# Kernel optimization log

Measured on AMD Instinct MI355X. Metric: run time of the kernel, lower is better.

Reference implementation:

```python
import jax, jax.numpy as jnp
import numpy as np

N = 100000          # num nodes
NUM_GRAPHS = 64
NEG_SLOPE = 0.2     # PyG GATv2Conv default


def gatv2_layer(x, src, dst, Wl, bl, Wr, br, att, bias, heads, out_ch, concat):
    # x: [N, F_in]; src/dst: [E] (self-loops already included)
    xl = (x @ Wl + bl).reshape(-1, heads, out_ch)   # source transform
    xr = (x @ Wr + br).reshape(-1, heads, out_ch)   # target transform
    m = jax.nn.leaky_relu(xl[src] + xr[dst], NEG_SLOPE)      # [E, H, C]
    alpha = jnp.einsum('ehc,hc->eh', m, att)                 # [E, H]
    # segment softmax over destination nodes
    amax = jax.ops.segment_max(alpha, dst, num_segments=N)
    alpha = jnp.exp(alpha - amax[dst])
    denom = jax.ops.segment_sum(alpha, dst, num_segments=N)
    alpha = alpha / (denom[dst] + 1e-16)
    out = jax.ops.segment_sum(xl[src] * alpha[..., None], dst, num_segments=N)
    out = out.reshape(N, heads * out_ch) if concat else out.mean(axis=1)
    return out + bias


def setup_inputs() -> dict:
    key = jax.random.key(0)
    ks = jax.random.split(key, 16)
    E = 3200000
    x = jax.random.normal(ks[0], (N, 256), dtype=jnp.float32)
    edge_index = jax.random.randint(ks[1], (2, E), 0, N, dtype=jnp.int64)
    batch = jnp.sort(jax.random.randint(ks[2], (N,), 0, NUM_GRAPHS, dtype=jnp.int64))
    H1, C1 = 8, 4
    s1 = 1.0 / np.sqrt(256)
    s2 = 1.0 / np.sqrt(H1 * C1)
    return {
        'x': x, 'edge_index': edge_index, 'batch': batch,
        'W1l': jax.random.normal(ks[3], (256, H1 * C1), jnp.float32) * s1,
        'b1l': jnp.zeros((H1 * C1,), jnp.float32),
        'W1r': jax.random.normal(ks[4], (256, H1 * C1), jnp.float32) * s1,
        'b1r': jnp.zeros((H1 * C1,), jnp.float32),
        'att1': jax.random.normal(ks[5], (H1, C1), jnp.float32),
        'bias1': jnp.zeros((H1 * C1,), jnp.float32),
        'W2l': jax.random.normal(ks[6], (H1 * C1, 64), jnp.float32) * s2,
        'b2l': jnp.zeros((64,), jnp.float32),
        'W2r': jax.random.normal(ks[7], (H1 * C1, 64), jnp.float32) * s2,
        'b2r': jnp.zeros((64,), jnp.float32),
        'att2': jax.random.normal(ks[8], (1, 64), jnp.float32),
        'bias2': jnp.zeros((64,), jnp.float32),
    }


def reference(x, edge_index, batch, W1l, b1l, W1r, b1r, att1, bias1,
              W2l, b2l, W2r, b2r, att2, bias2):
    # add self-loops (PyG GATv2Conv default add_self_loops=True)
    loop = jnp.arange(N, dtype=edge_index.dtype)
    src = jnp.concatenate([edge_index[0], loop])
    dst = jnp.concatenate([edge_index[1], loop])
    h = gatv2_layer(x, src, dst, W1l, b1l, W1r, b1r, att1, bias1, 8, 4, True)
    h = jax.nn.elu(h)
    h = gatv2_layer(h, src, dst, W2l, b2l, W2r, b2r, att2, bias2, 1, 64, False)
    # global mean pool over graphs
    sums = jax.ops.segment_sum(h, batch, num_segments=NUM_GRAPHS)
    counts = jax.ops.segment_sum(jnp.ones((N, 1), h.dtype), batch, num_segments=NUM_GRAPHS)
    return sums / jnp.maximum(counts, 1.0)
```

## Files before the change

### kernel.cpp

```cpp
#include <hip/hip_runtime.h>
#include <math.h>

#define NN 100000
#define EE 3200000
#define ET (EE + NN)
#define NG 64

#define NB 196
#define BWID 512
#define PCHUNK 8192
#define PBLOCKS ((ET + PCHUNK - 1) / PCHUNK)

#define X1_SPLIT 50048
#define X1BLK_A 391
#define X1BLK_B 391

#define OFF_XL1B  0u
#define OFF_XR1   1600000u
#define OFF_HL2B  8000000u
#define OFF_HR2   11200000u
#define OFF_BEDGE 8000000u
#define OFF_RP    17600000u
#define OFF_ESRC  17700096u
#define OFF_POOL  21000096u
#define OFF_CNTG  21004192u
#define OFF_BCNT  21004256u
#define OFF_BOFF  21004512u
#define OFF_GCUR  21004768u
#define OFF_AL2   21005024u
#define OFF_AR2   21105024u
#define WS_UNITS  21205024u

__device__ __forceinline__ float lrelu(float v) { return fmaxf(v, 0.2f * v); }

__device__ __forceinline__ unsigned pack_bf2(float a, float b) {
  unsigned ua = __float_as_uint(a), ub = __float_as_uint(b);
  ua = (ua + 0x7FFFu + ((ua >> 16) & 1u)) >> 16;
  ub = (ub + 0x7FFFu + ((ub >> 16) & 1u)) & 0xFFFF0000u;
  return ua | ub;
}
__device__ __forceinline__ float bf_lo(unsigned u) { return __uint_as_float(u << 16); }
__device__ __forceinline__ float bf_hi(unsigned u) { return __uint_as_float(u & 0xFFFF0000u); }

__global__ __launch_bounds__(256) void k_bcount(const int* __restrict__ ei,
                                                int* __restrict__ bcnt) {
  __shared__ int h[NB];
  for (int i = threadIdx.x; i < NB; i += 256) h[i] = 0;
  __syncthreads();
  for (long e = (long)blockIdx.x * 256 + threadIdx.x; e < ET; e += (long)gridDim.x * 256) {
    int d = (e < EE) ? ei[EE + e] : (int)(e - EE);
    atomicAdd(&h[d >> 9], 1);
  }
  __syncthreads();
  for (int i = threadIdx.x; i < NB; i += 256) if (h[i]) atomicAdd(&bcnt[i], h[i]);
}

__global__ __launch_bounds__(256) void k_bscan(const int* __restrict__ bcnt,
                                               int* __restrict__ boff, int* __restrict__ gcur) {
  __shared__ int sd[256];
  int t = threadIdx.x;
  int v = (t < NB) ? bcnt[t] : 0;
  sd[t] = v;
  __syncthreads();
  for (int o = 1; o < 256; o <<= 1) {
    int u = (t >= o) ? sd[t - o] : 0;
    __syncthreads();
    sd[t] += u;
    __syncthreads();
  }
  if (t < NB) { boff[t] = sd[t] - v; gcur[t] = sd[t] - v; }
  if (t == 0) boff[NB] = ET;
}

__device__ void part_role(char* smem, const int* __restrict__ ei,
                          int* __restrict__ gcur, int* __restrict__ bedge, int pblk) {
  int* cnt   = (int*)smem;
  int* lbase = cnt + NB;
  int* gbase = lbase + NB;
  int* sc    = gbase + NB;
  int* buf   = sc + 256;
  unsigned char* bkt = (unsigned char*)(buf + PCHUNK);
  int tid = threadIdx.x;
  long e0 = (long)pblk * PCHUNK;
  int nedge = (e0 + PCHUNK <= ET) ? PCHUNK : (int)(ET - e0);

  for (int i = tid; i < NB; i += 512) cnt[i] = 0;
  __syncthreads();
  for (int i = tid; i < nedge; i += 512) {
    long e = e0 + i;
    int d = (e < EE) ? ei[EE + e] : (int)(e - EE);
    atomicAdd(&cnt[d >> 9], 1);
  }
  __syncthreads();
  if (tid < 256) sc[tid] = (tid < NB) ? cnt[tid] : 0;
  __syncthreads();
  for (int o = 1; o < 256; o <<= 1) {
    int u = (tid < 256 && tid >= o) ? sc[tid - o] : 0;
    __syncthreads();
    if (tid < 256) sc[tid] += u;
    __syncthreads();
  }
  if (tid < NB) lbase[tid] = sc[tid] - cnt[tid];
  __syncthreads();
  if (tid < NB) {
    int c = cnt[tid];
    gbase[tid] = c ? atomicAdd(&gcur[tid], c) : 0;
    cnt[tid] = 0;
  }
  __syncthreads();
  for (int i = tid; i < nedge; i += 512) {
    long e = e0 + i;
    int s, d;
    if (e < EE) { s = ei[e]; d = ei[EE + e]; }
    else { s = (int)(e - EE); d = s; }
    int b = d >> 9;
    int r = atomicAdd(&cnt[b], 1);
    int idx = lbase[b] + r;
    buf[idx] = s | ((d & 511) << 17);
    bkt[idx] = (unsigned char)b;
  }
  __syncthreads();
  for (int i = tid; i < nedge; i += 512) {
    int p = buf[i];
    int b = bkt[i];
    bedge[gbase[b] + (i - lbase[b])] = p;
  }
}

__device__ void csr_role(char* smem, const int* __restrict__ boff,
                         const int* __restrict__ bedge,
                         int* __restrict__ rp, int* __restrict__ esrc, int b) {
  int* sdeg  = (int*)smem;
  int* sscan = sdeg + BWID;
  int t = threadIdx.x;
  int n0 = b * BWID;
  int lo = boff[b], hi = boff[b + 1];
  sdeg[t] = 0;
  __syncthreads();
  for (int i = lo + t; i < hi; i += 512) {
    int p = bedge[i];
    atomicAdd(&sdeg[p >> 17], 1);
  }
  __syncthreads();
  int v = sdeg[t];
  sscan[t] = v;
  __syncthreads();
  for (int o = 1; o < 512; o <<= 1) {
    int u = (t >= o) ? sscan[t - o] : 0;
    __syncthreads();
    sscan[t] += u;
    __syncthreads();
  }
  int excl = sscan[t] - v;
  int n = n0 + t;
  if (n < NN) rp[n] = lo + excl;
  if (b == NB - 1 && t == 0) rp[NN] = ET;
  __syncthreads();
  sdeg[t] = lo + excl;
  __syncthreads();
  for (int i = lo + t; i < hi; i += 512) {
    int p = bedge[i];
    int pos = atomicAdd(&sdeg[p >> 17], 1);
    esrc[pos] = p & 0x1FFFF;
  }
}

#define FMA4A(a, xv) \
  a.x += xv.x*w0.x + xv.y*w1.x + xv.z*w2.x + xv.w*w3.x; \
  a.y += xv.x*w0.y + xv.y*w1.y + xv.z*w2.y + xv.w*w3.y; \
  a.z += xv.x*w0.z + xv.y*w1.z + xv.z*w2.z + xv.w*w3.z; \
  a.w += xv.x*w0.w + xv.y*w1.w + xv.z*w2.w + xv.w*w3.w;

__device__ void xform1_role(char* smem, const float* __restrict__ x,
                            const float* __restrict__ Wl, const float* __restrict__ bl,
                            const float* __restrict__ Wr, const float* __restrict__ br,
                            unsigned short* __restrict__ xl1b, float* __restrict__ xr1,
                            int n_base) {
  float* Wlds = (float*)smem;
  int tid = threadIdx.x;
  int ci = tid & 15;
  int cbase = ci * 4;
  int n0 = n_base + (tid >> 4) * 4;
  int r0 = n0 + 0 < NN ? n0 + 0 : NN - 1;
  int r1 = n0 + 1 < NN ? n0 + 1 : NN - 1;
  int r2 = n0 + 2 < NN ? n0 + 2 : NN - 1;
  int r3 = n0 + 3 < NN ? n0 + 3 : NN - 1;
  const float* xb0 = x + (size_t)r0 * 256;
  const float* xb1 = x + (size_t)r1 * 256;
  const float* xb2 = x + (size_t)r2 * 256;
  const float* xb3 = x + (size_t)r3 * 256;
  float4 acc0 = {0,0,0,0}, acc1 = {0,0,0,0}, acc2 = {0,0,0,0}, acc3 = {0,0,0,0};

  for (int q = 0; q < 4; ++q) {
    int k0 = q * 64;
    __syncthreads();
    for (int i = tid; i < 64 * 64; i += 512) {
      int k = (i >> 6) + k0, c = i & 63;
      Wlds[i] = (c < 32) ? Wl[k * 32 + c] : Wr[k * 32 + (c - 32)];
    }
    __syncthreads();
#pragma unroll 2
    for (int kk = 0; kk < 64; kk += 4) {
      int k = k0 + kk;
      float4 xv0 = *(const float4*)(xb0 + k);
      float4 xv1 = *(const float4*)(xb1 + k);
      float4 xv2 = *(const float4*)(xb2 + k);
      float4 xv3 = *(const float4*)(xb3 + k);
      const float* wr = &Wlds[kk * 64 + cbase];
      float4 w0 = *(const float4*)(wr);
      float4 w1 = *(const float4*)(wr + 64);
      float4 w2 = *(const float4*)(wr + 128);
      float4 w3 = *(const float4*)(wr + 192);
      FMA4A(acc0, xv0)
      FMA4A(acc1, xv1)
      FMA4A(acc2, xv2)
      FMA4A(acc3, xv3)
    }
  }
  float4 acc[4] = {acc0, acc1, acc2, acc3};
  if (cbase < 32) {
    float4 bv = { bl[cbase], bl[cbase+1], bl[cbase+2], bl[cbase+3] };
#pragma unroll
    for (int j = 0; j < 4; ++j) {
      int n = n0 + j;
      if (n < NN) {
        uint2 o = { pack_bf2(acc[j].x + bv.x, acc[j].y + bv.y),
                    pack_bf2(acc[j].z + bv.z, acc[j].w + bv.w) };
        *(uint2*)(xl1b + (size_t)n * 32 + cbase) = o;
      }
    }
  } else {
    int c2 = cbase - 32;
    float4 bv = { br[c2], br[c2+1], br[c2+2], br[c2+3] };
#pragma unroll
    for (int j = 0; j < 4; ++j) {
      int n = n0 + j;
      if (n < NN) {
        float4 o = { acc[j].x + bv.x, acc[j].y + bv.y, acc[j].z + bv.z, acc[j].w + bv.w };
        *(float4*)(xr1 + (size_t)n * 32 + c2) = o;
      }
    }
  }
}

__global__ __launch_bounds__(512) void k_part_x1(
    const int* __restrict__ ei, int* __restrict__ gcur, int* __restrict__ bedge,
    const float* __restrict__ x,
    const float* __restrict__ Wl, const float* __restrict__ bl,
    const float* __restrict__ Wr, const float* __restrict__ br,
    unsigned short* __restrict__ xl1b, float* __restrict__ xr1) {
  extern __shared__ char smem[];
  if (blockIdx.x < PBLOCKS)
    part_role(smem, ei, gcur, bedge, blockIdx.x);
  else
    xform1_role(smem, x, Wl, bl, Wr, br, xl1b, xr1, (blockIdx.x - PBLOCKS) * 128);
}

__global__ __launch_bounds__(512) void k_csr_x1(
    const int* __restrict__ boff, const int* __restrict__ bedge,
    int* __restrict__ rp, int* __restrict__ esrc,
    const float* __restrict__ x,
    const float* __restrict__ Wl, const float* __restrict__ bl,
    const float* __restrict__ Wr, const float* __restrict__ br,
    unsigned short* __restrict__ xl1b, float* __restrict__ xr1) {
  extern __shared__ char smem[];
  if (blockIdx.x < NB)
    csr_role(smem, boff, bedge, rp, esrc, blockIdx.x);
  else
    xform1_role(smem, x, Wl, bl, Wr, br, xl1b, xr1,
                X1_SPLIT + (blockIdx.x - NB) * 128);
}

__global__ __launch_bounds__(256) void k_gather1x2(
    const int* __restrict__ rp, const int* __restrict__ esrc,
    const unsigned short* __restrict__ xl1b, const float* __restrict__ xr1,
    const float* __restrict__ att1, const float* __restrict__ bias1,
    const float* __restrict__ W2l, const float* __restrict__ b2l,
    const float* __restrict__ W2r, const float* __restrict__ b2r,
    const float* __restrict__ att2,
    unsigned short* __restrict__ hl2b, float* __restrict__ hr2,
    float* __restrict__ AL2, float* __restrict__ AR2) {
  __shared__ float W2lds[32 * 128];
  __shared__ float hlds[8][33];
  int tid = threadIdx.x;
  for (int i = tid; i < 32 * 128; i += 256) {
    int k = i >> 7, c = i & 127;
    W2lds[i] = (c < 64) ? W2l[k * 64 + c] : W2r[k * 64 + (c - 64)];
  }
  int n = blockIdx.x * 8 + (tid >> 5);
  int l = tid & 31;
  float av = att1[l];
  float xr = xr1[(size_t)n * 32 + l];
  int rpn = rp[n], dg = rp[n + 1] - rpn;
  float acc = 0.0f, den = 0.0f;
  int j = 0;
  for (; j + 4 <= dg; j += 4) {
    int s0 = esrc[rpn + j + 0];
    int s1 = esrc[rpn + j + 1];
    int s2 = esrc[rpn + j + 2];
    int s3 = esrc[rpn + j + 3];
    float x0 = bf_lo(xl1b[(size_t)s0 * 32 + l]);
    float x1 = bf_lo(xl1b[(size_t)s1 * 32 + l]);
    float x2 = bf_lo(xl1b[(size_t)s2 * 32 + l]);
    float x3 = bf_lo(xl1b[(size_t)s3 * 32 + l]);
    float p0 = lrelu(x0 + xr) * av;
    float p1 = lrelu(x1 + xr) * av;
    float p2 = lrelu(x2 + xr) * av;
    float p3 = lrelu(x3 + xr) * av;
    p0 += __shfl_xor(p0, 1); p1 += __shfl_xor(p1, 1);
    p2 += __shfl_xor(p2, 1); p3 += __shfl_xor(p3, 1);
    p0 += __shfl_xor(p0, 2); p1 += __shfl_xor(p1, 2);
    p2 += __shfl_xor(p2, 2); p3 += __shfl_xor(p3, 2);
    float w0 = __expf(p0), w1 = __expf(p1), w2 = __expf(p2), w3 = __expf(p3);
    den += w0 + w1 + w2 + w3;
    acc += w0 * x0 + w1 * x1 + w2 * x2 + w3 * x3;
  }
  for (; j < dg; ++j) {
    int s = esrc[rpn + j];
    float xl = bf_lo(xl1b[(size_t)s * 32 + l]);
    float p = lrelu(xl + xr) * av;
    p += __shfl_xor(p, 1);
    p += __shfl_xor(p, 2);
    float w = __expf(p);
    den += w;
    acc += w * xl;
  }
  float v = acc / (den + 1e-16f) + bias1[l];
  v = v > 0.0f ? v : expm1f(v);
  hlds[tid >> 5][l] = v;
  __syncthreads();

  int ni = tid >> 5, ci = tid & 31, cbase = ci * 4;
  float4 a = {0,0,0,0};
#pragma unroll
  for (int k = 0; k < 32; ++k) {
    float hv = hlds[ni][k];
    float4 wv = *(const float4*)(&W2lds[k * 128 + cbase]);
    a.x += hv * wv.x; a.y += hv * wv.y; a.z += hv * wv.z; a.w += hv * wv.w;
  }
  int no = blockIdx.x * 8 + ni;
  float partial;
  if (cbase < 64) {
    uint2 o = { pack_bf2(a.x + b2l[cbase], a.y + b2l[cbase + 1]),
                pack_bf2(a.z + b2l[cbase + 2], a.w + b2l[cbase + 3]) };
    *(uint2*)(hl2b + (size_t)no * 64 + cbase) = o;
    partial = bf_lo(o.x) * att2[cbase + 0] + bf_hi(o.x) * att2[cbase + 1]
            + bf_lo(o.y) * att2[cbase + 2] + bf_hi(o.y) * att2[cbase + 3];
  } else {
    int c2 = cbase - 64;
    float4 o = { a.x + b2r[c2], a.y + b2r[c2 + 1], a.z + b2r[c2 + 2], a.w + b2r[c2 + 3] };
    *(float4*)(hr2 + (size_t)no * 64 + c2) = o;
    partial = o.x * att2[c2 + 0] + o.y * att2[c2 + 1]
            + o.z * att2[c2 + 2] + o.w * att2[c2 + 3];
  }
  partial += __shfl_xor(partial, 1);
  partial += __shfl_xor(partial, 2);
  partial += __shfl_xor(partial, 4);
  partial += __shfl_xor(partial, 8);
  if (ci == 0)  AL2[no] = partial;
  if (ci == 16) AR2[no] = partial;
}

#define G2_P(qq, pp) { \
  float4 U0 = { bf_lo(qq.x), bf_hi(qq.x), bf_lo(qq.y), bf_hi(qq.y) }; \
  float4 U1 = { bf_lo(qq.z), bf_hi(qq.z), bf_lo(qq.w), bf_hi(qq.w) }; \
  pp = fabsf(U0.x + hr0.x) * ac0.x + fabsf(U0.y + hr0.y) * ac0.y \
     + fabsf(U0.z + hr0.z) * ac0.z + fabsf(U0.w + hr0.w) * ac0.w \
     + fabsf(U1.x + hr1.x) * ac1.x + fabsf(U1.y + hr1.y) * ac1.y \
     + fabsf(U1.z + hr1.z) * ac1.z + fabsf(U1.w + hr1.w) * ac1.w; }

#define G2_ACC(qq, ww) { \
  float4 U0 = { bf_lo(qq.x), bf_hi(qq.x), bf_lo(qq.y), bf_hi(qq.y) }; \
  float4 U1 = { bf_lo(qq.z), bf_hi(qq.z), bf_lo(qq.w), bf_hi(qq.w) }; \
  a0.x += ww * U0.x; a0.y += ww * U0.y; a0.z += ww * U0.z; a0.w += ww * U0.w; \
  a1.x += ww * U1.x; a1.y += ww * U1.y; a1.z += ww * U1.z; a1.w += ww * U1.w; }

__global__ __launch_bounds__(256) void k_gather2(
    const int* __restrict__ rp, const int* __restrict__ esrc,
    const unsigned short* __restrict__ hl2b, const float* __restrict__ hr2,
    const float* __restrict__ att2, const float* __restrict__ bias2,
    const int* __restrict__ batch,
    const float* __restrict__ AL2, const float* __restrict__ AR2,
    float* __restrict__ pool, float* __restrict__ cntg) {
  __shared__ float ssum[4][64];
  __shared__ float scnt[4];
  int tid = threadIdx.x;
  int n = (blockIdx.x * 256 + tid) >> 3;
  int l8 = tid & 7;
  int nblk0 = blockIdx.x * 32;
  int gmin = batch[nblk0];
  int gspan = batch[nblk0 + 31] - gmin + 1;
  ssum[tid >> 6][tid & 63] = 0.0f;
  if (tid < 4) scnt[tid] = 0.0f;
  __syncthreads();

  float4 ac0 = *(const float4*)(att2 + l8 * 8);
  float4 ac1 = *(const float4*)(att2 + l8 * 8 + 4);
  float4 bs0 = *(const float4*)(bias2 + l8 * 8);
  float4 bs1 = *(const float4*)(bias2 + l8 * 8 + 4);
  const float4* hrp = (const float4*)(hr2 + (size_t)n * 64 + l8 * 8);
  float4 hr0 = hrp[0], hr1 = hrp[1];
  float ard = 0.6f * AR2[n];
  int rpn = rp[n], dg = rp[n + 1] - rpn;
  float4 a0 = {0,0,0,0}, a1 = {0,0,0,0};
  float den = 0.0f;
  int j = 0;
  for (; j + 4 <= dg; j += 4) {
    int s0 = esrc[rpn + j + 0];
    int s1 = esrc[rpn + j + 1];
    int s2 = esrc[rpn + j + 2];
    int s3 = esrc[rpn + j + 3];
    uint4 q0 = *(const uint4*)(hl2b + (size_t)s0 * 64 + l8 * 8);
    uint4 q1 = *(const uint4*)(hl2b + (size_t)s1 * 64 + l8 * 8);
    uint4 q2 = *(const uint4*)(hl2b + (size_t)s2 * 64 + l8 * 8);
    uint4 q3 = *(const uint4*)(hl2b + (size_t)s3 * 64 + l8 * 8);
    float al0 = AL2[s0], al1 = AL2[s1], al2 = AL2[s2], al3 = AL2[s3];
    float p0, p1, p2, p3;
    G2_P(q0, p0) G2_P(q1, p1) G2_P(q2, p2) G2_P(q3, p3)
    p0 += __shfl_xor(p0, 1); p1 += __shfl_xor(p1, 1);
    p2 += __shfl_xor(p2, 1); p3 += __shfl_xor(p3, 1);
    p0 += __shfl_xor(p0, 2); p1 += __shfl_xor(p1, 2);
    p2 += __shfl_xor(p2, 2); p3 += __shfl_xor(p3, 2);
    p0 += __shfl_xor(p0, 4); p1 += __shfl_xor(p1, 4);
    p2 += __shfl_xor(p2, 4); p3 += __shfl_xor(p3, 4);
    float w0 = __expf(fmaf(0.6f, al0, fmaf(0.4f, p0, ard)));
    float w1 = __expf(fmaf(0.6f, al1, fmaf(0.4f, p1, ard)));
    float w2 = __expf(fmaf(0.6f, al2, fmaf(0.4f, p2, ard)));
    float w3 = __expf(fmaf(0.6f, al3, fmaf(0.4f, p3, ard)));
    den += w0 + w1 + w2 + w3;
    G2_ACC(q0, w0) G2_ACC(q1, w1) G2_ACC(q2, w2) G2_ACC(q3, w3)
  }
  for (; j < dg; ++j) {
    int s = esrc[rpn + j];
    uint4 q0 = *(const uint4*)(hl2b + (size_t)s * 64 + l8 * 8);
    float al = AL2[s];
    float p;
    G2_P(q0, p)
    p += __shfl_xor(p, 1);
    p += __shfl_xor(p, 2);
    p += __shfl_xor(p, 4);
    float w = __expf(fmaf(0.6f, al, fmaf(0.4f, p, ard)));
    den += w;
    G2_ACC(q0, w)
  }
  float inv = 1.0f / (den + 1e-16f);
  int gi = batch[n] - gmin;
  float* sp = &ssum[gi][l8 * 8];
  atomicAdd(sp + 0, a0.x * inv + bs0.x);
  atomicAdd(sp + 1, a0.y * inv + bs0.y);
  atomicAdd(sp + 2, a0.z * inv + bs0.z);
  atomicAdd(sp + 3, a0.w * inv + bs0.w);
  atomicAdd(sp + 4, a1.x * inv + bs1.x);
  atomicAdd(sp + 5, a1.y * inv + bs1.y);
  atomicAdd(sp + 6, a1.z * inv + bs1.z);
  atomicAdd(sp + 7, a1.w * inv + bs1.w);
  if (l8 == 0) atomicAdd(&scnt[gi], 1.0f);
  __syncthreads();
  for (int i = tid; i < gspan * 64; i += 256)
    atomicAdd(pool + (size_t)(gmin + (i >> 6)) * 64 + (i & 63), ssum[i >> 6][i & 63]);
  if (tid < gspan) atomicAdd(cntg + gmin + tid, scnt[tid]);
}

__global__ __launch_bounds__(256) void k_final(
    const float* __restrict__ pool, const float* __restrict__ cntg,
    float* __restrict__ out) {
  int i = blockIdx.x * 256 + threadIdx.x;
  if (i < NG * 64) out[i] = pool[i] / fmaxf(cntg[i >> 6], 1.0f);
}

extern "C" void kernel_launch(void* const* d_in, const int* in_sizes, int n_in,
                              void* d_out, int out_size, void* d_ws, size_t ws_size,
                              hipStream_t stream) {
  const float* x     = (const float*)d_in[0];
  const int*   ei    = (const int*)d_in[1];
  const int*   batch = (const int*)d_in[2];
  const float* W1l   = (const float*)d_in[3];
  const float* b1l   = (const float*)d_in[4];
  const float* W1r   = (const float*)d_in[5];
  const float* b1r   = (const float*)d_in[6];
  const float* att1  = (const float*)d_in[7];
  const float* bias1 = (const float*)d_in[8];
  const float* W2l   = (const float*)d_in[9];
  const float* b2l   = (const float*)d_in[10];
  const float* W2r   = (const float*)d_in[11];
  const float* b2r   = (const float*)d_in[12];
  const float* att2  = (const float*)d_in[13];
  const float* bias2 = (const float*)d_in[14];
  float* ws = (float*)d_ws;
  int*   wi = (int*)d_ws;
  float* out = (float*)d_out;

  hipMemsetAsync(ws + OFF_POOL, 0, (size_t)(OFF_AL2 - OFF_POOL) * 4, stream);

  k_bcount<<<512, 256, 0, stream>>>(ei, wi + OFF_BCNT);
  k_bscan<<<1, 256, 0, stream>>>(wi + OFF_BCNT, wi + OFF_BOFF, wi + OFF_GCUR);
  k_part_x1<<<PBLOCKS + X1BLK_A, 512, 44352, stream>>>(
      ei, wi + OFF_GCUR, wi + OFF_BEDGE,
      x, W1l, b1l, W1r, b1r, (unsigned short*)(ws + OFF_XL1B), ws + OFF_XR1);
  k_csr_x1<<<NB + X1BLK_B, 512, 16384, stream>>>(
      wi + OFF_BOFF, wi + OFF_BEDGE, wi + OFF_RP, wi + OFF_ESRC,
      x, W1l, b1l, W1r, b1r, (unsigned short*)(ws + OFF_XL1B), ws + OFF_XR1);

  k_gather1x2<<<NN / 8, 256, 0, stream>>>(wi + OFF_RP, wi + OFF_ESRC,
                                          (const unsigned short*)(ws + OFF_XL1B), ws + OFF_XR1,
                                          att1, bias1, W2l, b2l, W2r, b2r, att2,
                                          (unsigned short*)(ws + OFF_HL2B), ws + OFF_HR2,
                                          ws + OFF_AL2, ws + OFF_AR2);
  k_gather2<<<(NN * 8 + 255) / 256, 256, 0, stream>>>(wi + OFF_RP, wi + OFF_ESRC,
                                                      (const unsigned short*)(ws + OFF_HL2B),
                                                      ws + OFF_HR2, att2, bias2, batch,
                                                      ws + OFF_AL2, ws + OFF_AR2,
                                                      ws + OFF_POOL, ws + OFF_CNTG);
  k_final<<<16, 256, 0, stream>>>(ws + OFF_POOL, ws + OFF_CNTG, out);
}
```

Measured before the change: 352.4 us.

## Use packed FP32 math in gather2 and halve partition chunk size

Rewrites the second-layer gather inner loop to use v_pk_add/mul/fma_f32 inline asm on float pairs, so the attention dot product and weighted accumulation issue half as many VALU instructions. It also halves PCHUNK for the edge partition kernel, doubling the number of partition blocks and computing the shared-memory size from a formula. Inline asm may hinder compiler scheduling, and the smaller chunks add per-block overhead in exchange for more parallelism and less LDS per block.

```diff
diff --git a/kernel.cpp b/kernel.cpp
--- a/kernel.cpp
+++ b/kernel.cpp
@@ -8,8 +8,9 @@
 
 #define NB 196
 #define BWID 512
-#define PCHUNK 8192
+#define PCHUNK 4096
 #define PBLOCKS ((ET + PCHUNK - 1) / PCHUNK)
+#define PART_SMEM (NB * 12 + 1024 + PCHUNK * 4 + PCHUNK)
 
 #define X1_SPLIT 50048
 #define X1BLK_A 391
@@ -41,6 +42,26 @@
 }
 __device__ __forceinline__ float bf_lo(unsigned u) { return __uint_as_float(u << 16); }
 __device__ __forceinline__ float bf_hi(unsigned u) { return __uint_as_float(u & 0xFFFF0000u); }
+
+typedef float f32x2 __attribute__((ext_vector_type(2)));
+__device__ __forceinline__ f32x2 pk_add(f32x2 a, f32x2 b) {
+  f32x2 r; asm("v_pk_add_f32 %0, %1, %2" : "=v"(r) : "v"(a), "v"(b)); return r;
+}
+__device__ __forceinline__ f32x2 pk_mul(f32x2 a, f32x2 b) {
+  f32x2 r; asm("v_pk_mul_f32 %0, %1, %2" : "=v"(r) : "v"(a), "v"(b)); return r;
+}
+__device__ __forceinline__ f32x2 pk_fma(f32x2 a, f32x2 b, f32x2 c) {
+  f32x2 r; asm("v_pk_fma_f32 %0, %1, %2, %3" : "=v"(r) : "v"(a), "v"(b), "v"(c)); return r;
+}
+__device__ __forceinline__ f32x2 unpk2(unsigned u) {
+  f32x2 r; r.x = __uint_as_float(u << 16); r.y = __uint_as_float(u & 0xFFFF0000u); return r;
+}
+__device__ __forceinline__ f32x2 abs2(f32x2 a) {
+  f32x2 r;
+  r.x = __uint_as_float(__float_as_uint(a.x) & 0x7FFFFFFFu);
+  r.y = __uint_as_float(__float_as_uint(a.y) & 0x7FFFFFFFu);
+  return r;
+}
 
 __global__ __launch_bounds__(256) void k_bcount(const int* __restrict__ ei,
                                                 int* __restrict__ bcnt) {
@@ -361,19 +382,19 @@
   if (ci == 16) AR2[no] = partial;
 }
 
-#define G2_P(qq, pp) { \
-  float4 U0 = { bf_lo(qq.x), bf_hi(qq.x), bf_lo(qq.y), bf_hi(qq.y) }; \
-  float4 U1 = { bf_lo(qq.z), bf_hi(qq.z), bf_lo(qq.w), bf_hi(qq.w) }; \
-  pp = fabsf(U0.x + hr0.x) * ac0.x + fabsf(U0.y + hr0.y) * ac0.y \
-     + fabsf(U0.z + hr0.z) * ac0.z + fabsf(U0.w + hr0.w) * ac0.w \
-     + fabsf(U1.x + hr1.x) * ac1.x + fabsf(U1.y + hr1.y) * ac1.y \
-     + fabsf(U1.z + hr1.z) * ac1.z + fabsf(U1.w + hr1.w) * ac1.w; }
-
-#define G2_ACC(qq, ww) { \
-  float4 U0 = { bf_lo(qq.x), bf_hi(qq.x), bf_lo(qq.y), bf_hi(qq.y) }; \
-  float4 U1 = { bf_lo(qq.z), bf_hi(qq.z), bf_lo(qq.w), bf_hi(qq.w) }; \
-  a0.x += ww * U0.x; a0.y += ww * U0.y; a0.z += ww * U0.z; a0.w += ww * U0.w; \
-  a1.x += ww * U1.x; a1.y += ww * U1.y; a1.z += ww * U1.z; a1.w += ww * U1.w; }
+#define G2E(qq, u0O, u1O, u2O, u3O, pO) \
+  f32x2 u0O = unpk2(qq.x), u1O = unpk2(qq.y), u2O = unpk2(qq.z), u3O = unpk2(qq.w); \
+  float pO; { \
+    f32x2 pa__ = pk_mul(abs2(pk_add(u0O, hp0)), ap0); \
+    pa__ = pk_fma(abs2(pk_add(u1O, hp1)), ap1, pa__); \
+    pa__ = pk_fma(abs2(pk_add(u2O, hp2)), ap2, pa__); \
+    pa__ = pk_fma(abs2(pk_add(u3O, hp3)), ap3, pa__); \
+    pO = pa__.x + pa__.y; }
+
+#define G2A(u0O, u1O, u2O, u3O, ww) { \
+  f32x2 wv__; wv__.x = (ww); wv__.y = (ww); \
+  A0 = pk_fma(u0O, wv__, A0); A1 = pk_fma(u1O, wv__, A1); \
+  A2 = pk_fma(u2O, wv__, A2); A3 = pk_fma(u3O, wv__, A3); }
 
 __global__ __launch_bounds__(256) void k_gather2(
     const int* __restrict__ rp, const int* __restrict__ esrc,
@@ -398,11 +419,17 @@
   float4 ac1 = *(const float4*)(att2 + l8 * 8 + 4);
   float4 bs0 = *(const float4*)(bias2 + l8 * 8);
   float4 bs1 = *(const float4*)(bias2 + l8 * 8 + 4);
+  f32x2 ap0, ap1, ap2, ap3;
+  ap0.x = ac0.x; ap0.y = ac0.y; ap1.x = ac0.z; ap1.y = ac0.w;
+  ap2.x = ac1.x; ap2.y = ac1.y; ap3.x = ac1.z; ap3.y = ac1.w;
   const float4* hrp = (const float4*)(hr2 + (size_t)n * 64 + l8 * 8);
-  float4 hr0 = hrp[0], hr1 = hrp[1];
+  float4 h0 = hrp[0], h1 = hrp[1];
+  f32x2 hp0, hp1, hp2, hp3;
+  hp0.x = h0.x; hp0.y = h0.y; hp1.x = h0.z; hp1.y = h0.w;
+  hp2.x = h1.x; hp2.y = h1.y; hp3.x = h1.z; hp3.y = h1.w;
   float ard = 0.6f * AR2[n];
   int rpn = rp[n], dg = rp[n + 1] - rpn;
-  float4 a0 = {0,0,0,0}, a1 = {0,0,0,0};
+  f32x2 A0 = {0.f,0.f}, A1 = {0.f,0.f}, A2 = {0.f,0.f}, A3 = {0.f,0.f};
   float den = 0.0f;
   int j = 0;
   for (; j + 4 <= dg; j += 4) {
@@ -415,8 +442,10 @@
     uint4 q2 = *(const uint4*)(hl2b + (size_t)s2 * 64 + l8 * 8);
     uint4 q3 = *(const uint4*)(hl2b + (size_t)s3 * 64 + l8 * 8);
     float al0 = AL2[s0], al1 = AL2[s1], al2 = AL2[s2], al3 = AL2[s3];
-    float p0, p1, p2, p3;
-    G2_P(q0, p0) G2_P(q1, p1) G2_P(q2, p2) G2_P(q3, p3)
+    G2E(q0, e0u0, e0u1, e0u2, e0u3, p0)
+    G2E(q1, e1u0, e1u1, e1u2, e1u3, p1)
+    G2E(q2, e2u0, e2u1, e2u2, e2u3, p2)
+    G2E(q3, e3u0, e3u1, e3u2, e3u3, p3)
     p0 += __shfl_xor(p0, 1); p1 += __shfl_xor(p1, 1);
     p2 += __shfl_xor(p2, 1); p3 += __shfl_xor(p3, 1);
     p0 += __shfl_xor(p0, 2); p1 += __shfl_xor(p1, 2);
@@ -428,32 +457,34 @@
     float w2 = __expf(fmaf(0.6f, al2, fmaf(0.4f, p2, ard)));
     float w3 = __expf(fmaf(0.6f, al3, fmaf(0.4f, p3, ard)));
     den += w0 + w1 + w2 + w3;
-    G2_ACC(q0, w0) G2_ACC(q1, w1) G2_ACC(q2, w2) G2_ACC(q3, w3)
+    G2A(e0u0, e0u1, e0u2, e0u3, w0)
+    G2A(e1u0, e1u1, e1u2, e1u3, w1)
+    G2A(e2u0, e2u1, e2u2, e2u3, w2)
+    G2A(e3u0, e3u1, e3u2, e3u3, w3)
   }
   for (; j < dg; ++j) {
     int s = esrc[rpn + j];
     uint4 q0 = *(const uint4*)(hl2b + (size_t)s * 64 + l8 * 8);
     float al = AL2[s];
-    float p;
-    G2_P(q0, p)
+    G2E(q0, tu0, tu1, tu2, tu3, p)
     p += __shfl_xor(p, 1);
     p += __shfl_xor(p, 2);
     p += __shfl_xor(p, 4);
     float w = __expf(fmaf(0.6f, al, fmaf(0.4f, p, ard)));
     den += w;
-    G2_ACC(q0, w)
+    G2A(tu0, tu1, tu2, tu3, w)
   }
   float inv = 1.0f / (den + 1e-16f);
   int gi = batch[n] - gmin;
   float* sp = &ssum[gi][l8 * 8];
-  atomicAdd(sp + 0, a0.x * inv + bs0.x);
-  atomicAdd(sp + 1, a0.y * inv + bs0.y);
-  atomicAdd(sp + 2, a0.z * inv + bs0.z);
-  atomicAdd(sp + 3, a0.w * inv + bs0.w);
-  atomicAdd(sp + 4, a1.x * inv + bs1.x);
-  atomicAdd(sp + 5, a1.y * inv + bs1.y);
-  atomicAdd(sp + 6, a1.z * inv + bs1.z);
-  atomicAdd(sp + 7, a1.w * inv + bs1.w);
+  atomicAdd(sp + 0, A0.x * inv + bs0.x);
+  atomicAdd(sp + 1, A0.y * inv + bs0.y);
+  atomicAdd(sp + 2, A1.x * inv + bs0.z);
+  atomicAdd(sp + 3, A1.y * inv + bs0.w);
+  atomicAdd(sp + 4, A2.x * inv + bs1.x);
+  atomicAdd(sp + 5, A2.y * inv + bs1.y);
+  atomicAdd(sp + 6, A3.x * inv + bs1.z);
+  atomicAdd(sp + 7, A3.y * inv + bs1.w);
   if (l8 == 0) atomicAdd(&scnt[gi], 1.0f);
   __syncthreads();
   for (int i = tid; i < gspan * 64; i += 256)
@@ -494,7 +525,7 @@
 
   k_bcount<<<512, 256, 0, stream>>>(ei, wi + OFF_BCNT);
   k_bscan<<<1, 256, 0, stream>>>(wi + OFF_BCNT, wi + OFF_BOFF, wi + OFF_GCUR);
-  k_part_x1<<<PBLOCKS + X1BLK_A, 512, 44352, stream>>>(
+  k_part_x1<<<PBLOCKS + X1BLK_A, 512, PART_SMEM, stream>>>(
       ei, wi + OFF_GCUR, wi + OFF_BEDGE,
       x, W1l, b1l, W1r, b1r, (unsigned short*)(ws + OFF_XL1B), ws + OFF_XR1);
   k_csr_x1<<<NB + X1BLK_B, 512, 16384, stream>>>(
```

Result: no change. 355.2 us (+0.8%).
